# Performance work log

Hardware: AMD Instinct MI355X
Metric: run time of the kernel (lower is better)

Reference implementation:

```python
import jax, jax.numpy as jnp
import numpy as np


def l2norm(x, axis=-1, eps=1e-06):
    inv_norm = jax.lax.rsqrt(jnp.sum(x * x, axis=axis, keepdims=True) + eps)
    return x * inv_norm


def setup_inputs() -> dict:
    key0 = jax.random.key(0)
    ks = jax.random.split(key0, 5)
    B, S, H, Dk, Dv = 4, 2048, 16, 128, 128
    query = jax.random.normal(ks[0], (B, S, H, Dk), dtype=jnp.float32)
    key = jax.random.normal(ks[1], (B, S, H, Dk), dtype=jnp.float32)
    value = jax.random.normal(ks[2], (B, S, H, Dv), dtype=jnp.float32)
    # g is a log-decay: negative so decay = exp(g) in (exp(-1), 1)
    g = -jax.random.uniform(ks[3], (B, S, H), dtype=jnp.float32)
    # beta plays the role of sigmoid(.) mixing coefficient in (0, 1)
    beta = jax.random.uniform(ks[4], (B, S, H), dtype=jnp.float32)
    return {"query": query, "key": key, "value": value, "g": g, "beta": beta}


def reference(query, key, value, g, beta):
    # Gated delta-rule recurrence (Qwen3.5 GatedDeltaNet / recurrent_gated_delta_rule)
    dtype = query.dtype
    q = l2norm(query)
    k = l2norm(key)
    v = value
    scale = 1.0 / float(np.sqrt(q.shape[-1]))
    q = q * scale
    # time-major: [S, B, H, D]
    q = jnp.swapaxes(q, 0, 1)
    k = jnp.swapaxes(k, 0, 1)
    v = jnp.swapaxes(v, 0, 1)
    g_t = jnp.swapaxes(g, 0, 1)
    b_t = jnp.swapaxes(beta, 0, 1)
    B, H, Dk = q.shape[1], q.shape[2], q.shape[3]
    Dv = v.shape[3]
    init_state = jnp.zeros((B, H, Dk, Dv), dtype=dtype)

    def step_fn(state, inputs):
        q_i, k_i, v_i, g_i, beta_i = inputs
        decay = jnp.exp(g_i)[..., None, None]            # [B,H,1,1]
        state = state * decay                            # [B,H,Dk,Dv]
        kv_mem = jnp.sum(state * k_i[..., :, None], axis=-2)   # [B,H,Dv]
        delta = (v_i - kv_mem) * beta_i[..., None]              # [B,H,Dv]
        state = state + k_i[..., :, None] * delta[..., None, :]
        out_i = jnp.sum(state * q_i[..., :, None], axis=-2)    # [B,H,Dv]
        return state, out_i

    final_state, outputs = jax.lax.scan(step_fn, init_state, (q, k, v, g_t, b_t))
    outputs = jnp.swapaxes(outputs, 0, 1).astype(dtype)  # [B,S,H,Dv]
    return outputs, final_state.astype(dtype)
```

## Files before the change

### kernel.cpp

```cpp
#include <hip/hip_runtime.h>


#define Bsz 4
#define Ssz 2048
#define Hsz 16
#define Dsz 128

constexpr int ROWS = Bsz * Ssz * Hsz;
constexpr int VSTR = Hsz * Dsz;
constexpr float EPS = 1e-6f;
constexpr float SCALE = 0.08838834764831845f;

typedef float v2f __attribute__((ext_vector_type(2)));

template <int CTRL>
__device__ __forceinline__ float dpp_add(float x) {
  int y = __builtin_amdgcn_update_dpp(0, __float_as_int(x), CTRL, 0xF, 0xF, true);
  return x + __int_as_float(y);
}
__device__ __forceinline__ float reduce8(float x) {
  x = dpp_add<0xB1>(x);
  x = dpp_add<0x4E>(x);
  x = dpp_add<0x141>(x);
  return x;
}

__global__ __launch_bounds__(256) void prep_kernel(
    const float* __restrict__ q, const float* __restrict__ k,
    const float* __restrict__ g, const float* __restrict__ beta,
    float4* __restrict__ pack) {
  int r = blockIdx.x * 4 + (threadIdx.x >> 6);
  int lane = threadIdx.x & 63;
  const float2* q2p = reinterpret_cast<const float2*>(q + (size_t)r * Dsz);
  const float2* k2p = reinterpret_cast<const float2*>(k + (size_t)r * Dsz);
  float2 q2 = q2p[lane];
  float2 k2 = k2p[lane];
  float sq = fmaf(q2.x, q2.x, q2.y * q2.y);
  float sk = fmaf(k2.x, k2.x, k2.y * k2.y);
#pragma unroll
  for (int m = 1; m < 64; m <<= 1) {
    sq += __shfl_xor(sq, m, 64);
    sk += __shfl_xor(sk, m, 64);
  }
  if (lane == 0) {
    float xq = sq + EPS;
    float rq = rsqrtf(xq);
    rq = rq * (1.5f - 0.5f * xq * rq * rq);
    float xk = sk + EPS;
    float rk = rsqrtf(xk);
    rk = rk * (1.5f - 0.5f * xk * rk * rk);
    float dec = expf(g[r]);
    float bi = beta[r] * rk;
    int h = r % Hsz;
    int s = (r / Hsz) % Ssz;
    int b = r / (Hsz * Ssz);
    pack[(size_t)(b * Hsz + h) * Ssz + s] = make_float4(dec, rk, rq * SCALE, bi);
  }
}

#define DDEPTH 8
#define BATCH 4
#define SLOT_B 1280
#define WAVE_B (DDEPTH * SLOT_B)

__device__ __forceinline__ void dma16(unsigned long long g, unsigned int l) {
  __builtin_amdgcn_global_load_lds(
      (const __attribute__((address_space(1))) void*)g,
      (__attribute__((address_space(3))) void*)(unsigned long long)l, 16, 0, 0);
}
__device__ __forceinline__ void dma4(unsigned long long g, unsigned int l) {
  __builtin_amdgcn_global_load_lds(
      (const __attribute__((address_space(1))) void*)g,
      (__attribute__((address_space(3))) void*)(unsigned long long)l, 4, 0, 0);
}

struct BufP {
  v2f kr[8];
  v2f qr[8];
  float4 p;
  float vv;
};

__device__ __forceinline__ void ld_buf(BufP& b, const char* slot, int dkl, int dvg) {
  const float4* kp = (const float4*)(slot + dkl * 16);
#pragma unroll
  for (int r = 0; r < 4; ++r) {
    float4 kt = kp[r * 8];
    float4 qt = kp[r * 8 + 32];
    b.kr[2 * r] = (v2f){kt.x, kt.y};
    b.kr[2 * r + 1] = (v2f){kt.z, kt.w};
    b.qr[2 * r] = (v2f){qt.x, qt.y};
    b.qr[2 * r + 1] = (v2f){qt.z, qt.w};
  }
  b.vv = *(const float*)(slot + 1024 + dvg * 4);
  b.p = *(const float4*)(slot + 1056);
}

__device__ __forceinline__ float step_compute(const BufP& b, v2f (&st)[8]) {
  v2f a0 = st[0] * b.kr[0];
  v2f a1 = st[1] * b.kr[1];
#pragma unroll
  for (int i = 2; i < 8; i += 2) {
    a0 = __builtin_elementwise_fma(st[i], b.kr[i], a0);
    a1 = __builtin_elementwise_fma(st[i + 1], b.kr[i + 1], a1);
  }
  float acc = (a0.x + a0.y) + (a1.x + a1.y);
  acc = reduce8(acc);
  float dec = b.p.x;
  float kv = acc * dec * b.p.y;
  float dl = (b.vv - kv) * b.p.w;
  v2f dec2 = (v2f){dec, dec};
  v2f dl2 = (v2f){dl, dl};
  v2f o0 = (v2f){0.f, 0.f};
  v2f o1 = (v2f){0.f, 0.f};
#pragma unroll
  for (int i = 0; i < 8; i += 2) {
    st[i] = __builtin_elementwise_fma(st[i], dec2, b.kr[i] * dl2);
    st[i + 1] = __builtin_elementwise_fma(st[i + 1], dec2, b.kr[i + 1] * dl2);
    o0 = __builtin_elementwise_fma(st[i], b.qr[i], o0);
    o1 = __builtin_elementwise_fma(st[i + 1], b.qr[i + 1], o1);
  }
  float oacc = (o0.x + o0.y) + (o1.x + o1.y);
  oacc = reduce8(oacc);
  return oacc * b.p.z;
}

__global__ __launch_bounds__(256, 1) void scan_kernel(
    const float* __restrict__ q, const float* __restrict__ k,
    const float* __restrict__ v, const float4* __restrict__ pack,
    float* __restrict__ out, float* __restrict__ stateOut) {
  __shared__ __align__(16) char smem[4 * WAVE_B];

  const int blk = blockIdx.x;
  const int bh = blk & 63;
  const int chunk = blk >> 6;
  const int tid = threadIdx.x;
  const int lane = tid & 63;
  const int wid = __builtin_amdgcn_readfirstlane(tid >> 6);
  const int dkl = lane & 7;
  const int dvg = lane >> 3;
  const int dv = chunk * 32 + wid * 8 + dvg;
  const int d0 = dkl * 16;

  const size_t base = ((size_t)(bh >> 4) * Ssz * Hsz + (bh & 15)) * Dsz;
  const float4* pp = pack + (size_t)bh * Ssz;

  const unsigned int wb3 =
      (unsigned int)(unsigned long long)(void*)smem + (unsigned int)(wid * WAVE_B);
  const char* wbg = smem + wid * WAVE_B;

  const int li = lane & 31;
  const int fofs = (li & 7) * 16 + (li >> 3) * 4;
  unsigned long long kq_g =
      (unsigned long long)(uintptr_t)(((lane < 32) ? k : q) + base + fofs);
  unsigned long long vp_g;
  unsigned int vp_stride;
  if (lane < 8) {
    vp_g = (unsigned long long)(uintptr_t)(v + base + chunk * 32 + wid * 8 + lane);
    vp_stride = VSTR * 4;
  } else {
    int pc = (lane < 12) ? (lane - 8) : 0;
    vp_g = (unsigned long long)(uintptr_t)((const float*)pp + pc);
    vp_stride = 16;
  }

#pragma unroll
  for (int r = 0; r < DDEPTH; ++r) {
    dma16(kq_g, wb3 + r * SLOT_B);
    dma4(vp_g, wb3 + r * SLOT_B + 1024);
    kq_g += VSTR * 4;
    vp_g += vp_stride;
  }
  int nrow = DDEPTH;

  v2f st[8];
#pragma unroll
  for (int i = 0; i < 8; ++i) st[i] = (v2f){0.f, 0.f};

  float* outp = out + base + (size_t)dkl * VSTR + dv;
  float ocap = 0.f;
  BufP A, Bb;

  for (int sb = 0; sb < Ssz; sb += 2 * BATCH) {
#pragma unroll
    for (int half = 0; half < 2; ++half) {
      const int s0 = half * BATCH;
      asm volatile("s_waitcnt vmcnt(8)" ::: "memory");
      ld_buf(A, wbg + (s0 + 0) * SLOT_B, dkl, dvg);
      ld_buf(Bb, wbg + (s0 + 1) * SLOT_B, dkl, dvg);
      {
        float o = step_compute(A, st);
        ocap = (dkl == s0 + 0) ? o : ocap;
      }
      ld_buf(A, wbg + (s0 + 2) * SLOT_B, dkl, dvg);
      {
        float o = step_compute(Bb, st);
        ocap = (dkl == s0 + 1) ? o : ocap;
      }
      ld_buf(Bb, wbg + (s0 + 3) * SLOT_B, dkl, dvg);
      {
        float o = step_compute(A, st);
        ocap = (dkl == s0 + 2) ? o : ocap;
      }
      {
        float o = step_compute(Bb, st);
        ocap = (dkl == s0 + 3) ? o : ocap;
      }
      if (half == 1) {
        *outp = ocap;
        outp += 8 * VSTR;
      }
      asm volatile("s_waitcnt lgkmcnt(0)" ::: "memory");
#pragma unroll
      for (int j = 0; j < BATCH; ++j) {
        dma16(kq_g, wb3 + (s0 + j) * SLOT_B);
        dma4(vp_g, wb3 + (s0 + j) * SLOT_B + 1024);
        if (nrow < Ssz - 1) {
          kq_g += VSTR * 4;
          vp_g += vp_stride;
          ++nrow;
        }
      }
    }
  }

  float* sp = stateOut + ((size_t)bh * Dsz + d0) * Dsz + dv;
#pragma unroll
  for (int j = 0; j < 8; ++j) {
    sp[(2 * j) * Dsz] = st[j].x;
    sp[(2 * j + 1) * Dsz] = st[j].y;
  }
}

extern "C" void kernel_launch(void* const* d_in, const int* in_sizes, int n_in,
                              void* d_out, int out_size, void* d_ws, size_t ws_size,
                              hipStream_t stream) {
  const float* q = (const float*)d_in[0];
  const float* k = (const float*)d_in[1];
  const float* v = (const float*)d_in[2];
  const float* g = (const float*)d_in[3];
  const float* beta = (const float*)d_in[4];
  float* out = (float*)d_out;
  float* stateOut = out + (size_t)Bsz * Ssz * Hsz * Dsz;
  float4* pack = (float4*)d_ws;

  prep_kernel<<<ROWS / 4, 256, 0, stream>>>(q, k, g, beta, pack);
  scan_kernel<<<256, 256, 0, stream>>>(q, k, v, pack, out, stateOut);
}
```

Measured before the change: 769.8 us.

## Split Dk across 16 lanes and double scan grid to 512 blocks

The scan kernel now splits the Dk dimension over 16 lanes with 8 state elements each instead of 8 lanes with 16, and each wave covers 4 value columns, so the grid doubles to 512 blocks with occupancy 2. This shortens each lane's serial per-timestep work and puts more waves on each CU to hide the recurrence latency. In exchange, every reduction takes an extra DPP step and the shared-memory K/Q loads are duplicated across more waves. The prep kernel is also reworked to handle 4 rows per wave with 16-lane DPP reductions, and sched_barriers are added around the LDS reads.

```diff
diff --git a/kernel.cpp b/kernel.cpp
--- a/kernel.cpp
+++ b/kernel.cpp
@@ -18,10 +18,11 @@
   int y = __builtin_amdgcn_update_dpp(0, __float_as_int(x), CTRL, 0xF, 0xF, true);
   return x + __int_as_float(y);
 }
-__device__ __forceinline__ float reduce8(float x) {
+__device__ __forceinline__ float reduce16(float x) {
   x = dpp_add<0xB1>(x);
   x = dpp_add<0x4E>(x);
   x = dpp_add<0x141>(x);
+  x = dpp_add<0x140>(x);
   return x;
 }
 
@@ -29,20 +30,22 @@
     const float* __restrict__ q, const float* __restrict__ k,
     const float* __restrict__ g, const float* __restrict__ beta,
     float4* __restrict__ pack) {
-  int r = blockIdx.x * 4 + (threadIdx.x >> 6);
+  int wid = threadIdx.x >> 6;
   int lane = threadIdx.x & 63;
-  const float2* q2p = reinterpret_cast<const float2*>(q + (size_t)r * Dsz);
-  const float2* k2p = reinterpret_cast<const float2*>(k + (size_t)r * Dsz);
-  float2 q2 = q2p[lane];
-  float2 k2 = k2p[lane];
-  float sq = fmaf(q2.x, q2.x, q2.y * q2.y);
-  float sk = fmaf(k2.x, k2.x, k2.y * k2.y);
-#pragma unroll
-  for (int m = 1; m < 64; m <<= 1) {
-    sq += __shfl_xor(sq, m, 64);
-    sk += __shfl_xor(sk, m, 64);
-  }
-  if (lane == 0) {
+  int lg = lane & 15;
+  int rg = lane >> 4;
+  int r = blockIdx.x * 16 + wid * 4 + rg;
+  const float4* qp = reinterpret_cast<const float4*>(q + (size_t)r * Dsz);
+  const float4* kp = reinterpret_cast<const float4*>(k + (size_t)r * Dsz);
+  float4 qa = qp[lg * 2], qb = qp[lg * 2 + 1];
+  float4 ka = kp[lg * 2], kb = kp[lg * 2 + 1];
+  float sq = qa.x * qa.x + qa.y * qa.y + qa.z * qa.z + qa.w * qa.w +
+             qb.x * qb.x + qb.y * qb.y + qb.z * qb.z + qb.w * qb.w;
+  float sk = ka.x * ka.x + ka.y * ka.y + ka.z * ka.z + ka.w * ka.w +
+             kb.x * kb.x + kb.y * kb.y + kb.z * kb.z + kb.w * kb.w;
+  sq = reduce16(sq);
+  sk = reduce16(sk);
+  if (lg == 0) {
     float xq = sq + EPS;
     float rq = rsqrtf(xq);
     rq = rq * (1.5f - 0.5f * xq * rq * rq);
@@ -75,37 +78,37 @@
 }
 
 struct BufP {
-  v2f kr[8];
-  v2f qr[8];
+  v2f kr[4];
+  v2f qr[4];
   float4 p;
   float vv;
 };
 
 __device__ __forceinline__ void ld_buf(BufP& b, const char* slot, int dkl, int dvg) {
   const float4* kp = (const float4*)(slot + dkl * 16);
-#pragma unroll
-  for (int r = 0; r < 4; ++r) {
-    float4 kt = kp[r * 8];
-    float4 qt = kp[r * 8 + 32];
-    b.kr[2 * r] = (v2f){kt.x, kt.y};
-    b.kr[2 * r + 1] = (v2f){kt.z, kt.w};
-    b.qr[2 * r] = (v2f){qt.x, qt.y};
-    b.qr[2 * r + 1] = (v2f){qt.z, qt.w};
-  }
+  float4 k0 = kp[0];
+  float4 k1 = kp[16];
+  float4 q0 = kp[32];
+  float4 q1 = kp[48];
+  b.kr[0] = (v2f){k0.x, k0.y};
+  b.kr[1] = (v2f){k0.z, k0.w};
+  b.kr[2] = (v2f){k1.x, k1.y};
+  b.kr[3] = (v2f){k1.z, k1.w};
+  b.qr[0] = (v2f){q0.x, q0.y};
+  b.qr[1] = (v2f){q0.z, q0.w};
+  b.qr[2] = (v2f){q1.x, q1.y};
+  b.qr[3] = (v2f){q1.z, q1.w};
   b.vv = *(const float*)(slot + 1024 + dvg * 4);
-  b.p = *(const float4*)(slot + 1056);
-}
-
-__device__ __forceinline__ float step_compute(const BufP& b, v2f (&st)[8]) {
+  b.p = *(const float4*)(slot + 1040);
+}
+
+__device__ __forceinline__ float step_compute(const BufP& b, v2f (&st)[4]) {
   v2f a0 = st[0] * b.kr[0];
   v2f a1 = st[1] * b.kr[1];
-#pragma unroll
-  for (int i = 2; i < 8; i += 2) {
-    a0 = __builtin_elementwise_fma(st[i], b.kr[i], a0);
-    a1 = __builtin_elementwise_fma(st[i + 1], b.kr[i + 1], a1);
-  }
+  a0 = __builtin_elementwise_fma(st[2], b.kr[2], a0);
+  a1 = __builtin_elementwise_fma(st[3], b.kr[3], a1);
   float acc = (a0.x + a0.y) + (a1.x + a1.y);
-  acc = reduce8(acc);
+  acc = reduce16(acc);
   float dec = b.p.x;
   float kv = acc * dec * b.p.y;
   float dl = (b.vv - kv) * b.p.w;
@@ -114,18 +117,18 @@
   v2f o0 = (v2f){0.f, 0.f};
   v2f o1 = (v2f){0.f, 0.f};
 #pragma unroll
-  for (int i = 0; i < 8; i += 2) {
+  for (int i = 0; i < 4; i += 2) {
     st[i] = __builtin_elementwise_fma(st[i], dec2, b.kr[i] * dl2);
     st[i + 1] = __builtin_elementwise_fma(st[i + 1], dec2, b.kr[i + 1] * dl2);
     o0 = __builtin_elementwise_fma(st[i], b.qr[i], o0);
     o1 = __builtin_elementwise_fma(st[i + 1], b.qr[i + 1], o1);
   }
   float oacc = (o0.x + o0.y) + (o1.x + o1.y);
-  oacc = reduce8(oacc);
+  oacc = reduce16(oacc);
   return oacc * b.p.z;
 }
 
-__global__ __launch_bounds__(256, 1) void scan_kernel(
+__global__ __launch_bounds__(256, 2) void scan_kernel(
     const float* __restrict__ q, const float* __restrict__ k,
     const float* __restrict__ v, const float4* __restrict__ pack,
     float* __restrict__ out, float* __restrict__ stateOut) {
@@ -133,14 +136,13 @@
 
   const int blk = blockIdx.x;
   const int bh = blk & 63;
-  const int chunk = blk >> 6;
+  const int cc = blk >> 6;
   const int tid = threadIdx.x;
   const int lane = tid & 63;
   const int wid = __builtin_amdgcn_readfirstlane(tid >> 6);
-  const int dkl = lane & 7;
-  const int dvg = lane >> 3;
-  const int dv = chunk * 32 + wid * 8 + dvg;
-  const int d0 = dkl * 16;
+  const int dkl = lane & 15;
+  const int dvg = lane >> 4;
+  const int dv = cc * 16 + wid * 4 + dvg;
 
   const size_t base = ((size_t)(bh >> 4) * Ssz * Hsz + (bh & 15)) * Dsz;
   const float4* pp = pack + (size_t)bh * Ssz;
@@ -150,16 +152,16 @@
   const char* wbg = smem + wid * WAVE_B;
 
   const int li = lane & 31;
-  const int fofs = (li & 7) * 16 + (li >> 3) * 4;
+  const int fofs = (li < 16) ? (8 * li) : (8 * (li - 16) + 4);
   unsigned long long kq_g =
       (unsigned long long)(uintptr_t)(((lane < 32) ? k : q) + base + fofs);
   unsigned long long vp_g;
   unsigned int vp_stride;
-  if (lane < 8) {
-    vp_g = (unsigned long long)(uintptr_t)(v + base + chunk * 32 + wid * 8 + lane);
+  if (lane < 4) {
+    vp_g = (unsigned long long)(uintptr_t)(v + base + cc * 16 + wid * 4 + lane);
     vp_stride = VSTR * 4;
   } else {
-    int pc = (lane < 12) ? (lane - 8) : 0;
+    int pc = (lane < 8) ? (lane - 4) : 0;
     vp_g = (unsigned long long)(uintptr_t)((const float*)pp + pc);
     vp_stride = 16;
   }
@@ -173,42 +175,46 @@
   }
   int nrow = DDEPTH;
 
-  v2f st[8];
-#pragma unroll
-  for (int i = 0; i < 8; ++i) st[i] = (v2f){0.f, 0.f};
+  v2f st[4];
+#pragma unroll
+  for (int i = 0; i < 4; ++i) st[i] = (v2f){0.f, 0.f};
 
   float* outp = out + base + (size_t)dkl * VSTR + dv;
   float ocap = 0.f;
   BufP A, Bb;
 
-  for (int sb = 0; sb < Ssz; sb += 2 * BATCH) {
-#pragma unroll
-    for (int half = 0; half < 2; ++half) {
-      const int s0 = half * BATCH;
+  for (int sb = 0; sb < Ssz; sb += 16) {
+#pragma unroll
+    for (int gg = 0; gg < 4; ++gg) {
+      const int s0 = (gg & 1) * BATCH;
       asm volatile("s_waitcnt vmcnt(8)" ::: "memory");
       ld_buf(A, wbg + (s0 + 0) * SLOT_B, dkl, dvg);
+      __builtin_amdgcn_sched_barrier(0);
       ld_buf(Bb, wbg + (s0 + 1) * SLOT_B, dkl, dvg);
+      __builtin_amdgcn_sched_barrier(0);
       {
         float o = step_compute(A, st);
-        ocap = (dkl == s0 + 0) ? o : ocap;
+        ocap = (dkl == gg * 4 + 0) ? o : ocap;
       }
       ld_buf(A, wbg + (s0 + 2) * SLOT_B, dkl, dvg);
+      __builtin_amdgcn_sched_barrier(0);
       {
         float o = step_compute(Bb, st);
-        ocap = (dkl == s0 + 1) ? o : ocap;
+        ocap = (dkl == gg * 4 + 1) ? o : ocap;
       }
       ld_buf(Bb, wbg + (s0 + 3) * SLOT_B, dkl, dvg);
+      __builtin_amdgcn_sched_barrier(0);
       {
         float o = step_compute(A, st);
-        ocap = (dkl == s0 + 2) ? o : ocap;
+        ocap = (dkl == gg * 4 + 2) ? o : ocap;
       }
       {
         float o = step_compute(Bb, st);
-        ocap = (dkl == s0 + 3) ? o : ocap;
-      }
-      if (half == 1) {
+        ocap = (dkl == gg * 4 + 3) ? o : ocap;
+      }
+      if (gg == 3) {
         *outp = ocap;
-        outp += 8 * VSTR;
+        outp += 16 * VSTR;
       }
       asm volatile("s_waitcnt lgkmcnt(0)" ::: "memory");
 #pragma unroll
@@ -224,9 +230,9 @@
     }
   }
 
-  float* sp = stateOut + ((size_t)bh * Dsz + d0) * Dsz + dv;
-#pragma unroll
-  for (int j = 0; j < 8; ++j) {
+  float* sp = stateOut + ((size_t)bh * Dsz + dkl * 8) * Dsz + dv;
+#pragma unroll
+  for (int j = 0; j < 4; ++j) {
     sp[(2 * j) * Dsz] = st[j].x;
     sp[(2 * j + 1) * Dsz] = st[j].y;
   }
@@ -244,6 +250,6 @@
   float* stateOut = out + (size_t)Bsz * Ssz * Hsz * Dsz;
   float4* pack = (float4*)d_ws;
 
-  prep_kernel<<<ROWS / 4, 256, 0, stream>>>(q, k, g, beta, pack);
-  scan_kernel<<<256, 256, 0, stream>>>(q, k, v, pack, out, stateOut);
-}
+  prep_kernel<<<ROWS / 16, 256, 0, stream>>>(q, k, g, beta, pack);
+  scan_kernel<<<512, 256, 0, stream>>>(q, k, v, pack, out, stateOut);
+}
```

New measurement: 717.7 us. 6.8% less time.
